# Kernel optimization log

Hardware: AMD Instinct MI355X
Metric: run time of the kernel (lower is better)

The kernel has to match this reference:

```python
import jax, jax.numpy as jnp
import numpy as np

N_NODES = 100000
N_EDGES = 1600000
D_IN = 128
D_OUT = 128


def setup_inputs() -> dict:
    key = jax.random.key(0)
    k_x, k_e, k_wl, k_bl, k_wr = jax.random.split(key, 5)
    x = jax.random.normal(k_x, (N_NODES, D_IN), dtype=jnp.float32)
    edge_index = jax.random.randint(k_e, (2, N_EDGES), 0, N_NODES, dtype=jnp.int64)
    s = 1.0 / np.sqrt(D_IN)
    W_l = jax.random.uniform(k_wl, (D_OUT, D_IN), minval=-s, maxval=s, dtype=jnp.float32)
    b_l = jax.random.uniform(k_bl, (D_OUT,), minval=-s, maxval=s, dtype=jnp.float32)
    W_r = jax.random.uniform(k_wr, (D_OUT, D_IN), minval=-s, maxval=s, dtype=jnp.float32)
    return {"x": x, "edge_index": edge_index, "W_l": W_l, "b_l": b_l, "W_r": W_r}


def reference(x, edge_index, W_l, b_l, W_r):
    # PyG SAGEConv with mean aggregation:
    #   out = lin_l(mean_{j in N(i)} x_j) + lin_r(x_i), followed by ReLU.
    src, dst = edge_index[0], edge_index[1]
    # gather source features [E, D_IN] and mean-aggregate at destinations
    msg_sum = jax.ops.segment_sum(x[src], dst, num_segments=N_NODES)  # [N, D_IN]
    deg = jax.ops.segment_sum(jnp.ones((edge_index.shape[1],), dtype=x.dtype), dst,
                              num_segments=N_NODES)  # [N]
    agg = msg_sum / jnp.maximum(deg, 1.0)[:, None]  # isolated nodes -> 0
    out = agg @ W_l.T + b_l + x @ W_r.T
    return jax.nn.relu(out)
```

## Files before the change

### kernel.cpp

```cpp
#include <hip/hip_runtime.h>
#include <hip/hip_bf16.h>
#include <cstddef>
#include <cstdint>

#define D 128
#define BCAP 262144
#define BCHUNK 4096
#define SLOTS 64
#define TILE 128
#define LROW 68
#define SBCAP 5120
#define GPGMAX 64

typedef __bf16 bf16x8 __attribute__((ext_vector_type(8)));
typedef float  f32x4  __attribute__((ext_vector_type(4)));
typedef float  f32x2  __attribute__((ext_vector_type(2)));

__device__ __forceinline__ unsigned int f2bf(float f) {
    unsigned int u = __float_as_uint(f);
    return (u + 0x7FFFu + ((u >> 16) & 1u)) >> 16;
}

__global__ __launch_bounds__(256) void bucketx_kernel(
    const int* __restrict__ ei, int E, int* __restrict__ bucketCnt,
    int2* __restrict__ buckets, int nbBucket, int nbX,
    const float4* __restrict__ x4, uint2* __restrict__ xb2,
    unsigned int* __restrict__ xg, int nq,
    const float* __restrict__ Wl, const float* __restrict__ Wr,
    const float* __restrict__ bl, unsigned short* __restrict__ bfrag,
    float* __restrict__ biasbuf)
{
    const int bid = blockIdx.x;
    if (bid >= nbBucket) {
        const int xi = bid - nbBucket;
        if (xi < nbX) {
            const int base = xi * 1024 + threadIdx.x;
            #pragma unroll
            for (int k = 0; k < 4; k++) {
                int i = base + k * 256;
                if (i < nq) {
                    float4 v = x4[i];
                    uint2 r;
                    r.x = f2bf(v.x) | (f2bf(v.y) << 16);
                    r.y = f2bf(v.z) | (f2bf(v.w) << 16);
                    xb2[i] = r;
                    int g = 0;
                    g = __builtin_amdgcn_cvt_pk_fp8_f32(v.x, v.y, g, false);
                    g = __builtin_amdgcn_cvt_pk_fp8_f32(v.z, v.w, g, true);
                    xg[(size_t)((i >> 5) + 1) * 32 + (i & 31)] = (unsigned int)g;
                }
            }
        } else {
            int f = (xi - nbX) * 256 + threadIdx.x;
            if (f < 4096) {
                int ct   = f >> 9;
                int q    = (f >> 6) & 7;
                int lane = f & 63;
                int o  = 16 * ct + (lane & 15);
                int kb = 32 * q + (lane >> 4) * 8;
                const float* s = (kb < 128) ? (Wl + (size_t)o * 128 + kb)
                                            : (Wr + (size_t)o * 128 + (kb - 128));
                uint4 u;
                u.x = f2bf(s[0]) | (f2bf(s[1]) << 16);
                u.y = f2bf(s[2]) | (f2bf(s[3]) << 16);
                u.z = f2bf(s[4]) | (f2bf(s[5]) << 16);
                u.w = f2bf(s[6]) | (f2bf(s[7]) << 16);
                reinterpret_cast<uint4*>(bfrag)[f] = u;
                if (f < 128) biasbuf[f] = bl[f];
                if (f < 32)  xg[f] = 0u;
            }
        }
        return;
    }
    __shared__ int cnt[8], base[8], pos[8];
    const int cb  = bid * BCHUNK;
    const int end = min(cb + BCHUNK, E);
    if (threadIdx.x < 8) { cnt[threadIdx.x] = 0; pos[threadIdx.x] = 0; }
    __syncthreads();
    int srcs[16], dsts[16];
    #pragma unroll
    for (int k = 0; k < 16; k++) {
        int e = cb + threadIdx.x + k * 256;
        bool v = e < end;
        srcs[k] = v ? ei[e] : 0;
        dsts[k] = v ? ei[E + e] : -1;
        if (v) atomicAdd(&cnt[(dsts[k] >> 8) & 7], 1);
    }
    __syncthreads();
    if (threadIdx.x < 8)
        base[threadIdx.x] = atomicAdd(&bucketCnt[threadIdx.x], cnt[threadIdx.x]);
    __syncthreads();
    #pragma unroll
    for (int k = 0; k < 16; k++) {
        if (dsts[k] >= 0) {
            int p = (dsts[k] >> 8) & 7;
            int o = base[p] + atomicAdd(&pos[p], 1);
            if (o < BCAP) buckets[(size_t)p * BCAP + o] = make_int2(srcs[k], dsts[k]);
        }
    }
}

__global__ __launch_bounds__(256) void granule_kernel(
    const int2* __restrict__ buckets, const int* __restrict__ bucketCnt,
    int* __restrict__ subCnt, unsigned int* __restrict__ sub, int GPG)
{
    __shared__ int cnt[GPGMAX], base[GPGMAX], posl[GPGMAX];
    const int p = blockIdx.x & 7;
    const int j = blockIdx.x >> 3;
    const int n = min(bucketCnt[p], BCAP);
    const int lo = j * 4096;
    if (lo >= n) return;
    const int hi = min(lo + 4096, n);
    for (int i = threadIdx.x; i < GPG; i += 256) { cnt[i] = 0; posl[i] = 0; }
    __syncthreads();
    const int2* B = buckets + (size_t)p * BCAP;
    int2 e[16]; int gi[16];
    #pragma unroll
    for (int k = 0; k < 16; k++) {
        int i = lo + threadIdx.x + k * 256;
        bool v = i < hi;
        e[k] = v ? B[i] : make_int2(0, 0);
        gi[k] = v ? (e[k].y >> 11) : -1;
        if (v) atomicAdd(&cnt[gi[k]], 1);
    }
    __syncthreads();
    for (int i = threadIdx.x; i < GPG; i += 256)
        base[i] = (cnt[i] > 0) ? atomicAdd(&subCnt[p * GPG + i], cnt[i]) : 0;
    __syncthreads();
    #pragma unroll
    for (int k = 0; k < 16; k++) {
        if (gi[k] >= 0) {
            int pos = base[gi[k]] + atomicAdd(&posl[gi[k]], 1);
            if (pos < SBCAP)
                sub[(size_t)(p * GPG + gi[k]) * SBCAP + pos] =
                    (unsigned int)(e[k].x + 1) | ((unsigned int)(e[k].y & 255) << 20);
        }
    }
}

__global__ __launch_bounds__(256) void csrg_kernel(
    const unsigned int* __restrict__ sub, const int* __restrict__ subCnt,
    int* __restrict__ csr, int* __restrict__ deg, int GPG, int N)
{
    __shared__ int lcnt[256];
    const int g  = blockIdx.x;
    const int p  = g & 7;
    const int gi = g >> 3;
    const int sb = p * GPG + gi;
    const int n  = min(subCnt[sb], SBCAP);
    lcnt[threadIdx.x] = 0;
    __syncthreads();
    const unsigned int* S = sub + (size_t)sb * SBCAP;
    const int nbase = g << 8;
    for (int i = threadIdx.x; i < n; i += 256) {
        unsigned int en = S[i];
        int d8  = (en >> 20) & 255;
        int pos = atomicAdd(&lcnt[d8], 1);
        if (pos < SLOTS)
            csr[(size_t)(nbase + d8) * SLOTS + pos] = (int)(en & 0xFFFFFu);
    }
    __syncthreads();
    int node = nbase + threadIdx.x;
    if (node < N) deg[node] = lcnt[threadIdx.x];
}

__global__ __launch_bounds__(512) void gathformer_kernel(
    const int* __restrict__ deg_, const int* __restrict__ csr,
    const unsigned int* __restrict__ xg, const unsigned int* __restrict__ xb,
    const unsigned short* __restrict__ bfrag, const float* __restrict__ biasbuf,
    float* __restrict__ out, int N)
{
    __shared__ unsigned int lds[TILE * LROW];

    const int w    = threadIdx.x >> 6;
    const int lane = threadIdx.x & 63;
    const int sub  = lane & 31;
    const int half = lane >> 5;
    const int node0 = blockIdx.x * TILE;

    for (int i = 0; i < 16; i++) {
        int node = node0 + w * 16 + i;
        if (node >= N) break;
        int deg = deg_[node];
        int dl  = min(deg, SLOTS);
        int nbatch = (dl + 15) >> 4;
        const int* nb = csr + (size_t)node * SLOTS;
        f32x2 a01 = {0.f, 0.f};
        f32x2 a23 = {0.f, 0.f};
        for (int b = 0; b < nbatch; b++) {
            const int j = b * 16;
            unsigned int v[8];
            #pragma unroll
            for (int u = 0; u < 8; u++) {
                int slot = j + 2 * u + half;
                int raw  = nb[slot];
                int s    = (slot < dl) ? raw : 0;
                v[u] = xg[(size_t)s * 32 + sub];
            }
            #pragma unroll
            for (int u = 0; u < 8; u++) {
                a01 += __builtin_amdgcn_cvt_pk_f32_fp8(v[u], false);
                a23 += __builtin_amdgcn_cvt_pk_f32_fp8(v[u], true);
            }
        }
        a01.x += __shfl_xor(a01.x, 32);
        a01.y += __shfl_xor(a01.y, 32);
        a23.x += __shfl_xor(a23.x, 32);
        a23.y += __shfl_xor(a23.y, 32);
        if (half == 0) {
            float inv = 1.0f / fmaxf((float)deg, 1.0f);
            int b = (w * 16 + i) * LROW + sub * 2;
            lds[b]     = f2bf(a01.x * inv) | (f2bf(a01.y * inv) << 16);
            lds[b + 1] = f2bf(a23.x * inv) | (f2bf(a23.y * inv) << 16);
        }
    }
    __syncthreads();

    const int quad = lane >> 4;
    const int r15  = lane & 15;
    bf16x8 bw[8];
    #pragma unroll
    for (int q = 0; q < 8; q++)
        bw[q] = reinterpret_cast<const bf16x8*>(bfrag)[(w * 8 + q) * 64 + lane];
    const float bias = biasbuf[16 * w + r15];
    const int col = 16 * w + r15;

    #pragma unroll 1
    for (int mt = 0; mt < 8; mt++) {
        int rowbase = node0 + mt * 16;
        if (rowbase >= N) break;
        int rc = min(rowbase + r15, N - 1);
        f32x4 acc = {0.f, 0.f, 0.f, 0.f};
        const int lbase = (mt * 16 + r15) * LROW + quad * 4;
        #pragma unroll
        for (int q = 0; q < 4; q++) {
            bf16x8 a = *reinterpret_cast<const bf16x8*>(&lds[lbase + q * 16]);
            acc = __builtin_amdgcn_mfma_f32_16x16x32_bf16(a, bw[q], acc, 0, 0, 0);
        }
        const unsigned short* xrow =
            (const unsigned short*)xb + (size_t)rc * 128 + quad * 8;
        #pragma unroll
        for (int q = 4; q < 8; q++) {
            bf16x8 a = *reinterpret_cast<const bf16x8*>(xrow + (q - 4) * 32);
            acc = __builtin_amdgcn_mfma_f32_16x16x32_bf16(a, bw[q], acc, 0, 0, 0);
        }
        #pragma unroll
        for (int r = 0; r < 4; r++) {
            int orow = rowbase + quad * 4 + r;
            if (orow < N)
                out[(size_t)orow * D + col] = fmaxf(acc[r] + bias, 0.0f);
        }
    }
}

extern "C" void kernel_launch(void* const* d_in, const int* in_sizes, int n_in,
                              void* d_out, int out_size, void* d_ws, size_t ws_size,
                              hipStream_t stream)
{
    const float* x  = (const float*)d_in[0];
    const int*   ei = (const int*)d_in[1];
    const float* Wl = (const float*)d_in[2];
    const float* bl = (const float*)d_in[3];
    const float* Wr = (const float*)d_in[4];
    float* out = (float*)d_out;

    const int nodes = in_sizes[0] / D;
    const int E     = in_sizes[1] / 2;
    const int NG    = (nodes + 255) >> 8;
    const int GPG   = (NG + 7) >> 3;

    int* deg         = (int*)d_ws;
    unsigned int* xg = (unsigned int*)(deg + nodes);
    int* csr         = (int*)(xg + (size_t)(nodes + 1) * 32);
    unsigned int* xb = (unsigned int*)(csr + (size_t)nodes * SLOTS);
    unsigned short* bfrag = (unsigned short*)(xb + (size_t)nodes * 64);
    float* biasbuf   = (float*)(bfrag + 4096 * 8);
    int* bucketCnt   = (int*)(biasbuf + 128);
    int* subCnt      = bucketCnt + 8;
    int2* buckets    = (int2*)d_out;
    unsigned int* sub = (unsigned int*)((char*)d_out + (size_t)8 * BCAP * 8);

    hipMemsetAsync(bucketCnt, 0, (size_t)(8 + 8 * GPG) * sizeof(int), stream);

    const int nbBucket = (E + BCHUNK - 1) / BCHUNK;
    const int nq  = nodes * 32;
    const int nbX = (nq + 1023) / 1024;
    bucketx_kernel<<<nbBucket + nbX + 16, 256, 0, stream>>>(
        ei, E, bucketCnt, buckets, nbBucket, nbX,
        (const float4*)x, (uint2*)xb, xg, nq, Wl, Wr, bl, bfrag, biasbuf);

    const int PB = (BCAP + 4095) / 4096;
    granule_kernel<<<8 * PB, 256, 0, stream>>>(buckets, bucketCnt, subCnt, sub, GPG);

    csrg_kernel<<<NG, 256, 0, stream>>>(sub, subCnt, csr, deg, GPG, nodes);

    gathformer_kernel<<<(nodes + TILE - 1) / TILE, 512, 0, stream>>>(
        deg, csr, xg, xb, bfrag, biasbuf, out, nodes);
}
```

Measured before the change: 221.3 us.

## Software-pipeline neighbor gathers and stage self-features in swizzled LDS

The fused gather+GEMM kernel now loads each wave's CSR rows once per lane and broadcasts neighbor indices with shuffles. Gathers for the next node are double-buffered so they are in flight while the previous node is reduced. The bf16 self-feature tile is prefetched into LDS up front, and both the aggregate and self tiles use an XOR-swizzled layout to avoid bank conflicts. The cost is higher register pressure (two 16-entry gather buffers, with launch bounds set to 4 blocks) and twice the LDS footprint. Nodes with more than 32 neighbors fall back to an unpipelined extra pass.

New measurement: 221.5 us. Within noise of the previous version (+0.1%).

```diff
diff --git a/kernel.cpp b/kernel.cpp
--- a/kernel.cpp
+++ b/kernel.cpp
@@ -8,7 +8,7 @@
 #define BCHUNK 4096
 #define SLOTS 64
 #define TILE 128
-#define LROW 68
+#define XBASE 8192
 #define SBCAP 5120
 #define GPGMAX 64
 
@@ -164,13 +164,59 @@
     if (node < N) deg[node] = lcnt[threadIdx.x];
 }
 
-__global__ __launch_bounds__(512) void gathformer_kernel(
+__device__ __forceinline__ void gather_issue(
+    unsigned int (&vv)[16], int raw, int dl, int half, int sub,
+    const unsigned int* __restrict__ xg)
+{
+    #pragma unroll
+    for (int u = 0; u < 16; u++) {
+        int slot = 2 * u + half;
+        int s = (slot < dl) ? __shfl(raw, slot) : 0;
+        vv[u] = xg[(size_t)s * 32 + sub];
+    }
+}
+
+__device__ __forceinline__ void acc_reduce_write(
+    const unsigned int (&vv)[16], int raw, int dl, int dT, int row,
+    int half, int sub, const unsigned int* __restrict__ xg, unsigned int* lds)
+{
+    f32x2 a01 = {0.f, 0.f};
+    f32x2 a23 = {0.f, 0.f};
+    #pragma unroll
+    for (int u = 0; u < 16; u++) {
+        a01 += __builtin_amdgcn_cvt_pk_f32_fp8(vv[u], false);
+        a23 += __builtin_amdgcn_cvt_pk_f32_fp8(vv[u], true);
+    }
+    if (dl > 32) {
+        #pragma unroll
+        for (int u = 0; u < 16; u++) {
+            int slot = 32 + 2 * u + half;
+            int s = (slot < dl) ? __shfl(raw, slot) : 0;
+            unsigned int vt = xg[(size_t)s * 32 + sub];
+            a01 += __builtin_amdgcn_cvt_pk_f32_fp8(vt, false);
+            a23 += __builtin_amdgcn_cvt_pk_f32_fp8(vt, true);
+        }
+    }
+    a01.x += __shfl_xor(a01.x, 32);
+    a01.y += __shfl_xor(a01.y, 32);
+    a23.x += __shfl_xor(a23.x, 32);
+    a23.y += __shfl_xor(a23.y, 32);
+    if (half == 0) {
+        float inv = 1.0f / fmaxf((float)dT, 1.0f);
+        int ch   = (sub >> 1) ^ (row & 7);
+        int bofs = row * 64 + ch * 4 + (sub & 1) * 2;
+        lds[bofs]     = f2bf(a01.x * inv) | (f2bf(a01.y * inv) << 16);
+        lds[bofs + 1] = f2bf(a23.x * inv) | (f2bf(a23.y * inv) << 16);
+    }
+}
+
+__global__ __launch_bounds__(512, 4) void gathformer_kernel(
     const int* __restrict__ deg_, const int* __restrict__ csr,
     const unsigned int* __restrict__ xg, const unsigned int* __restrict__ xb,
     const unsigned short* __restrict__ bfrag, const float* __restrict__ biasbuf,
     float* __restrict__ out, int N)
 {
-    __shared__ unsigned int lds[TILE * LROW];
+    __shared__ unsigned int lds[2 * TILE * 64];
 
     const int w    = threadIdx.x >> 6;
     const int lane = threadIdx.x & 63;
@@ -178,43 +224,51 @@
     const int half = lane >> 5;
     const int node0 = blockIdx.x * TILE;
 
-    for (int i = 0; i < 16; i++) {
-        int node = node0 + w * 16 + i;
-        if (node >= N) break;
-        int deg = deg_[node];
-        int dl  = min(deg, SLOTS);
-        int nbatch = (dl + 15) >> 4;
-        const int* nb = csr + (size_t)node * SLOTS;
-        f32x2 a01 = {0.f, 0.f};
-        f32x2 a23 = {0.f, 0.f};
-        for (int b = 0; b < nbatch; b++) {
-            const int j = b * 16;
-            unsigned int v[8];
-            #pragma unroll
-            for (int u = 0; u < 8; u++) {
-                int slot = j + 2 * u + half;
-                int raw  = nb[slot];
-                int s    = (slot < dl) ? raw : 0;
-                v[u] = xg[(size_t)s * 32 + sub];
-            }
-            #pragma unroll
-            for (int u = 0; u < 8; u++) {
-                a01 += __builtin_amdgcn_cvt_pk_f32_fp8(v[u], false);
-                a23 += __builtin_amdgcn_cvt_pk_f32_fp8(v[u], true);
-            }
-        }
-        a01.x += __shfl_xor(a01.x, 32);
-        a01.y += __shfl_xor(a01.y, 32);
-        a23.x += __shfl_xor(a23.x, 32);
-        a23.y += __shfl_xor(a23.y, 32);
-        if (half == 0) {
-            float inv = 1.0f / fmaxf((float)deg, 1.0f);
-            int b = (w * 16 + i) * LROW + sub * 2;
-            lds[b]     = f2bf(a01.x * inv) | (f2bf(a01.y * inv) << 16);
-            lds[b + 1] = f2bf(a23.x * inv) | (f2bf(a23.y * inv) << 16);
-        }
-    }
-    __syncthreads();
+    uint4 xs[4];
+    const uint4* xb4 = reinterpret_cast<const uint4*>(xb);
+    #pragma unroll
+    for (int k = 0; k < 4; k++) {
+        int idx = k * 512 + (int)threadIdx.x;
+        int row = idx >> 4;
+        int gr  = min(node0 + row, N - 1);
+        xs[k] = xb4[(size_t)gr * 16 + (idx & 15)];
+    }
+
+    const int nb0 = node0 + w * 16;
+    int degv = 0;
+    if (lane < 16) {
+        int nd = nb0 + lane;
+        if (nd < N) degv = deg_[nd];
+    }
+    int r0 = csr[(size_t)min(nb0 + 0, N - 1) * SLOTS + lane];
+    int r1 = csr[(size_t)min(nb0 + 1, N - 1) * SLOTS + lane];
+    int r2 = csr[(size_t)min(nb0 + 2, N - 1) * SLOTS + lane];
+
+    #pragma unroll
+    for (int k = 0; k < 4; k++) {
+        int idx = k * 512 + (int)threadIdx.x;
+        int row = idx >> 4;
+        int cw  = (idx & 15) ^ (row & 7);
+        *reinterpret_cast<uint4*>(&lds[XBASE + row * 64 + cw * 4]) = xs[k];
+    }
+
+    unsigned int vA[16], vB[16];
+    int dl0 = min(__shfl(degv, 0), SLOTS);
+    gather_issue(vA, r0, dl0, half, sub, xg);
+    #pragma unroll
+    for (int i = 0; i < 16; i += 2) {
+        int dl1 = min(__shfl(degv, i + 1), SLOTS);
+        gather_issue(vB, r1, dl1, half, sub, xg);
+        int r3 = (i + 3 < 16) ? csr[(size_t)min(nb0 + i + 3, N - 1) * SLOTS + lane] : 0;
+        int dT0 = __shfl(degv, i);
+        acc_reduce_write(vA, r0, dl0, dT0, w * 16 + i, half, sub, xg, lds);
+        dl0 = (i + 2 < 16) ? min(__shfl(degv, i + 2), SLOTS) : 0;
+        if (i + 2 < 16) gather_issue(vA, r2, dl0, half, sub, xg);
+        int r4 = (i + 4 < 16) ? csr[(size_t)min(nb0 + i + 4, N - 1) * SLOTS + lane] : 0;
+        int dT1 = __shfl(degv, i + 1);
+        acc_reduce_write(vB, r1, dl1, dT1, w * 16 + i + 1, half, sub, xg, lds);
+        r0 = r2; r1 = r3; r2 = r4;
+    }
 
     const int quad = lane >> 4;
     const int r15  = lane & 15;
@@ -225,30 +279,33 @@
     const float bias = biasbuf[16 * w + r15];
     const int col = 16 * w + r15;
 
-    #pragma unroll 1
+    __syncthreads();
+
+    #pragma unroll 2
     for (int mt = 0; mt < 8; mt++) {
         int rowbase = node0 + mt * 16;
         if (rowbase >= N) break;
-        int rc = min(rowbase + r15, N - 1);
         f32x4 acc = {0.f, 0.f, 0.f, 0.f};
-        const int lbase = (mt * 16 + r15) * LROW + quad * 4;
+        const int r     = mt * 16 + r15;
+        const int rbase = r * 64;
+        const int rx    = r & 7;
         #pragma unroll
         for (int q = 0; q < 4; q++) {
-            bf16x8 a = *reinterpret_cast<const bf16x8*>(&lds[lbase + q * 16]);
+            int ch = (quad + 4 * q) ^ rx;
+            bf16x8 a = *reinterpret_cast<const bf16x8*>(&lds[rbase + ch * 4]);
             acc = __builtin_amdgcn_mfma_f32_16x16x32_bf16(a, bw[q], acc, 0, 0, 0);
         }
-        const unsigned short* xrow =
-            (const unsigned short*)xb + (size_t)rc * 128 + quad * 8;
         #pragma unroll
-        for (int q = 4; q < 8; q++) {
-            bf16x8 a = *reinterpret_cast<const bf16x8*>(xrow + (q - 4) * 32);
-            acc = __builtin_amdgcn_mfma_f32_16x16x32_bf16(a, bw[q], acc, 0, 0, 0);
+        for (int q = 0; q < 4; q++) {
+            int ch = (quad + 4 * q) ^ rx;
+            bf16x8 a = *reinterpret_cast<const bf16x8*>(&lds[XBASE + rbase + ch * 4]);
+            acc = __builtin_amdgcn_mfma_f32_16x16x32_bf16(a, bw[4 + q], acc, 0, 0, 0);
         }
         #pragma unroll
-        for (int r = 0; r < 4; r++) {
-            int orow = rowbase + quad * 4 + r;
+        for (int rr = 0; rr < 4; rr++) {
+            int orow = rowbase + quad * 4 + rr;
             if (orow < N)
-                out[(size_t)orow * D + col] = fmaxf(acc[r] + bias, 0.0f);
+                out[(size_t)orow * D + col] = fmaxf(acc[rr] + bias, 0.0f);
         }
     }
 }
```

## Collapse two-level edge bucketing into single-pass scatter to 256-node granules

Applied to the files above, without the earlier changes.

The edge bucketing kernel now scatters each edge straight into one of NG per-256-node sub-buckets using a shared-memory histogram of NG counters. This removes the intermediate 8-way bucket array and the separate granule kernel, so edges are written and read from global memory one fewer time and one launch goes away. In exchange each block keeps up to 512 shared counters and its writes are spread across about 391 destinations instead of 8, which lowers write coalescing and increases global atomic traffic on subCnt.

After: 222.3 us. About the same (+0.5%).

```diff
diff --git a/kernel.cpp b/kernel.cpp
--- a/kernel.cpp
+++ b/kernel.cpp
@@ -4,13 +4,12 @@
 #include <cstdint>
 
 #define D 128
-#define BCAP 262144
 #define BCHUNK 4096
 #define SLOTS 64
 #define TILE 128
 #define LROW 68
 #define SBCAP 5120
-#define GPGMAX 64
+#define NGMAX 512
 
 typedef __bf16 bf16x8 __attribute__((ext_vector_type(8)));
 typedef float  f32x4  __attribute__((ext_vector_type(4)));
@@ -21,9 +20,9 @@
     return (u + 0x7FFFu + ((u >> 16) & 1u)) >> 16;
 }
 
-__global__ __launch_bounds__(256) void bucketx_kernel(
-    const int* __restrict__ ei, int E, int* __restrict__ bucketCnt,
-    int2* __restrict__ buckets, int nbBucket, int nbX,
+__global__ __launch_bounds__(256) void bucketx2_kernel(
+    const int* __restrict__ ei, int E, int* __restrict__ subCnt,
+    unsigned int* __restrict__ sub, int NG, int nbE, int nbX,
     const float4* __restrict__ x4, uint2* __restrict__ xb2,
     unsigned int* __restrict__ xg, int nq,
     const float* __restrict__ Wl, const float* __restrict__ Wr,
@@ -31,8 +30,8 @@
     float* __restrict__ biasbuf)
 {
     const int bid = blockIdx.x;
-    if (bid >= nbBucket) {
-        const int xi = bid - nbBucket;
+    if (bid >= nbE) {
+        const int xi = bid - nbE;
         if (xi < nbX) {
             const int base = xi * 1024 + threadIdx.x;
             #pragma unroll
@@ -72,85 +71,46 @@
         }
         return;
     }
-    __shared__ int cnt[8], base[8], pos[8];
-    const int cb  = bid * BCHUNK;
-    const int end = min(cb + BCHUNK, E);
-    if (threadIdx.x < 8) { cnt[threadIdx.x] = 0; pos[threadIdx.x] = 0; }
-    __syncthreads();
-    int srcs[16], dsts[16];
+    __shared__ int cnt[NGMAX], base[NGMAX], posl[NGMAX];
+    for (int i = threadIdx.x; i < NG; i += 256) { cnt[i] = 0; posl[i] = 0; }
+    __syncthreads();
+    const int cb = bid * BCHUNK;
+    int srcs[16], gs[16], d8s[16];
     #pragma unroll
     for (int k = 0; k < 16; k++) {
         int e = cb + threadIdx.x + k * 256;
-        bool v = e < end;
+        bool v = e < E;
         srcs[k] = v ? ei[e] : 0;
-        dsts[k] = v ? ei[E + e] : -1;
-        if (v) atomicAdd(&cnt[(dsts[k] >> 8) & 7], 1);
-    }
-    __syncthreads();
-    if (threadIdx.x < 8)
-        base[threadIdx.x] = atomicAdd(&bucketCnt[threadIdx.x], cnt[threadIdx.x]);
+        int dst = v ? ei[E + e] : 0;
+        gs[k]  = v ? (dst >> 8) : -1;
+        d8s[k] = dst & 255;
+        if (v) atomicAdd(&cnt[gs[k]], 1);
+    }
+    __syncthreads();
+    for (int i = threadIdx.x; i < NG; i += 256)
+        base[i] = (cnt[i] > 0) ? atomicAdd(&subCnt[i], cnt[i]) : 0;
     __syncthreads();
     #pragma unroll
     for (int k = 0; k < 16; k++) {
-        if (dsts[k] >= 0) {
-            int p = (dsts[k] >> 8) & 7;
-            int o = base[p] + atomicAdd(&pos[p], 1);
-            if (o < BCAP) buckets[(size_t)p * BCAP + o] = make_int2(srcs[k], dsts[k]);
-        }
-    }
-}
-
-__global__ __launch_bounds__(256) void granule_kernel(
-    const int2* __restrict__ buckets, const int* __restrict__ bucketCnt,
-    int* __restrict__ subCnt, unsigned int* __restrict__ sub, int GPG)
-{
-    __shared__ int cnt[GPGMAX], base[GPGMAX], posl[GPGMAX];
-    const int p = blockIdx.x & 7;
-    const int j = blockIdx.x >> 3;
-    const int n = min(bucketCnt[p], BCAP);
-    const int lo = j * 4096;
-    if (lo >= n) return;
-    const int hi = min(lo + 4096, n);
-    for (int i = threadIdx.x; i < GPG; i += 256) { cnt[i] = 0; posl[i] = 0; }
-    __syncthreads();
-    const int2* B = buckets + (size_t)p * BCAP;
-    int2 e[16]; int gi[16];
-    #pragma unroll
-    for (int k = 0; k < 16; k++) {
-        int i = lo + threadIdx.x + k * 256;
-        bool v = i < hi;
-        e[k] = v ? B[i] : make_int2(0, 0);
-        gi[k] = v ? (e[k].y >> 11) : -1;
-        if (v) atomicAdd(&cnt[gi[k]], 1);
-    }
-    __syncthreads();
-    for (int i = threadIdx.x; i < GPG; i += 256)
-        base[i] = (cnt[i] > 0) ? atomicAdd(&subCnt[p * GPG + i], cnt[i]) : 0;
-    __syncthreads();
-    #pragma unroll
-    for (int k = 0; k < 16; k++) {
-        if (gi[k] >= 0) {
-            int pos = base[gi[k]] + atomicAdd(&posl[gi[k]], 1);
+        if (gs[k] >= 0) {
+            int pos = base[gs[k]] + atomicAdd(&posl[gs[k]], 1);
             if (pos < SBCAP)
-                sub[(size_t)(p * GPG + gi[k]) * SBCAP + pos] =
-                    (unsigned int)(e[k].x + 1) | ((unsigned int)(e[k].y & 255) << 20);
+                sub[(size_t)gs[k] * SBCAP + pos] =
+                    (unsigned int)(srcs[k] + 1) | ((unsigned int)d8s[k] << 20);
         }
     }
 }
 
 __global__ __launch_bounds__(256) void csrg_kernel(
     const unsigned int* __restrict__ sub, const int* __restrict__ subCnt,
-    int* __restrict__ csr, int* __restrict__ deg, int GPG, int N)
+    int* __restrict__ csr, int* __restrict__ deg, int N)
 {
     __shared__ int lcnt[256];
-    const int g  = blockIdx.x;
-    const int p  = g & 7;
-    const int gi = g >> 3;
-    const int sb = p * GPG + gi;
-    const int n  = min(subCnt[sb], SBCAP);
+    const int g = blockIdx.x;
+    const int n = min(subCnt[g], SBCAP);
     lcnt[threadIdx.x] = 0;
     __syncthreads();
-    const unsigned int* S = sub + (size_t)sb * SBCAP;
+    const unsigned int* S = sub + (size_t)g * SBCAP;
     const int nbase = g << 8;
     for (int i = threadIdx.x; i < n; i += 256) {
         unsigned int en = S[i];
@@ -267,7 +227,6 @@
     const int nodes = in_sizes[0] / D;
     const int E     = in_sizes[1] / 2;
     const int NG    = (nodes + 255) >> 8;
-    const int GPG   = (NG + 7) >> 3;
 
     int* deg         = (int*)d_ws;
     unsigned int* xg = (unsigned int*)(deg + nodes);
@@ -275,24 +234,19 @@
     unsigned int* xb = (unsigned int*)(csr + (size_t)nodes * SLOTS);
     unsigned short* bfrag = (unsigned short*)(xb + (size_t)nodes * 64);
     float* biasbuf   = (float*)(bfrag + 4096 * 8);
-    int* bucketCnt   = (int*)(biasbuf + 128);
-    int* subCnt      = bucketCnt + 8;
-    int2* buckets    = (int2*)d_out;
-    unsigned int* sub = (unsigned int*)((char*)d_out + (size_t)8 * BCAP * 8);
-
-    hipMemsetAsync(bucketCnt, 0, (size_t)(8 + 8 * GPG) * sizeof(int), stream);
-
-    const int nbBucket = (E + BCHUNK - 1) / BCHUNK;
+    int* subCnt      = (int*)(biasbuf + 128);
+    unsigned int* sub = (unsigned int*)d_out;
+
+    hipMemsetAsync(subCnt, 0, (size_t)NG * sizeof(int), stream);
+
+    const int nbE = (E + BCHUNK - 1) / BCHUNK;
     const int nq  = nodes * 32;
     const int nbX = (nq + 1023) / 1024;
-    bucketx_kernel<<<nbBucket + nbX + 16, 256, 0, stream>>>(
-        ei, E, bucketCnt, buckets, nbBucket, nbX,
+    bucketx2_kernel<<<nbE + nbX + 16, 256, 0, stream>>>(
+        ei, E, subCnt, sub, NG, nbE, nbX,
         (const float4*)x, (uint2*)xb, xg, nq, Wl, Wr, bl, bfrag, biasbuf);
 
-    const int PB = (BCAP + 4095) / 4096;
-    granule_kernel<<<8 * PB, 256, 0, stream>>>(buckets, bucketCnt, subCnt, sub, GPG);
-
-    csrg_kernel<<<NG, 256, 0, stream>>>(sub, subCnt, csr, deg, GPG, nodes);
+    csrg_kernel<<<NG, 256, 0, stream>>>(sub, subCnt, csr, deg, nodes);
 
     gathformer_kernel<<<(nodes + TILE - 1) / TILE, 512, 0, stream>>>(
         deg, csr, xg, xb, bfrag, biasbuf, out, nodes);
```
